# Kernel tuning notes

Measured on AMD Instinct MI355X. Metric: run time of the kernel, lower is better.

## Reference

```python
import jax, jax.numpy as jnp
import numpy as np

NUM_HEADS = 32
NUM_KV_HEADS = 8
HEAD_DIM = 128


def rotate_half(x):
    half = x.shape[-1] // 2
    return jnp.concatenate([-x[..., half:], x[..., :half]], axis=-1)


def setup_inputs() -> dict:
    key = jax.random.key(0)
    ks = jax.random.split(key, 7)
    B, S, H = 2, 2048, 4096
    hidden_states = jax.random.normal(ks[0], (B, S, H), dtype=jnp.float32)
    # rope tables built from real frequencies for realism
    inv_freq = 1.0 / (10000.0 ** (jnp.arange(0, HEAD_DIM, 2, dtype=jnp.float32) / HEAD_DIM))
    pos = jnp.arange(S, dtype=jnp.float32)
    freqs = pos[:, None] * inv_freq[None, :]            # [S, HEAD_DIM//2]
    emb = jnp.concatenate([freqs, freqs], axis=-1)      # [S, HEAD_DIM]
    cos = jnp.broadcast_to(jnp.cos(emb)[None], (B, S, HEAD_DIM)).astype(jnp.float32)
    sin = jnp.broadcast_to(jnp.sin(emb)[None], (B, S, HEAD_DIM)).astype(jnp.float32)
    scale = 0.02
    wq = jax.random.normal(ks[1], (NUM_HEADS * HEAD_DIM, H), dtype=jnp.float32) * scale
    wk = jax.random.normal(ks[2], (NUM_KV_HEADS * HEAD_DIM, H), dtype=jnp.float32) * scale
    wv = jax.random.normal(ks[3], (NUM_KV_HEADS * HEAD_DIM, H), dtype=jnp.float32) * scale
    wo = jax.random.normal(ks[4], (H, NUM_HEADS * HEAD_DIM), dtype=jnp.float32) * scale
    return {"hidden_states": hidden_states, "cos": cos, "sin": sin,
            "wq": wq, "wk": wk, "wv": wv, "wo": wo}


def reference(hidden_states, cos, sin, wq, wk, wv, wo):
    B, S, H = hidden_states.shape
    groups = NUM_HEADS // NUM_KV_HEADS
    scaling = HEAD_DIM ** -0.5

    # QKV projections (nn.Linear, no bias -> x @ W^T)
    q = (hidden_states @ wq.T).reshape(B, S, NUM_HEADS, HEAD_DIM).transpose(0, 2, 1, 3)     # [B,Hq,S,D]
    k = (hidden_states @ wk.T).reshape(B, S, NUM_KV_HEADS, HEAD_DIM).transpose(0, 2, 1, 3)  # [B,Hk,S,D]
    v = (hidden_states @ wv.T).reshape(B, S, NUM_KV_HEADS, HEAD_DIM).transpose(0, 2, 1, 3)  # [B,Hk,S,D]

    # RoPE (HF apply_rotary_pos_emb: cos/sin unsqueezed over head axis)
    c = cos[:, None, :, :]  # [B,1,S,D]
    s = sin[:, None, :, :]
    q = q * c + rotate_half(q) * s
    k = k * c + rotate_half(k) * s

    # GQA: broadcast each KV head to its group of query heads
    k = jnp.repeat(k, groups, axis=1)  # [B,Hq,S,D]
    v = jnp.repeat(v, groups, axis=1)

    # causal SDPA
    scores = jnp.einsum('bhqd,bhkd->bhqk', q, k) * scaling
    causal = jnp.tril(jnp.ones((S, S), dtype=bool))
    neg = jnp.finfo(scores.dtype).min
    scores = jnp.where(causal[None, None], scores, neg)
    probs = jax.nn.softmax(scores, axis=-1)
    attn = jnp.einsum('bhqk,bhkd->bhqd', probs, v)      # [B,Hq,S,D]

    # merge heads + output projection
    attn = attn.transpose(0, 2, 1, 3).reshape(B, S, NUM_HEADS * HEAD_DIM)
    return attn @ wo.T
```

## Files before the change

kernel.cpp:

```cpp
#include <hip/hip_runtime.h>
#include <stdint.h>

typedef __bf16 bf16_t;
typedef __bf16 bf16x8 __attribute__((ext_vector_type(8)));
typedef __bf16 bf16x4 __attribute__((ext_vector_type(4)));
typedef float f32x4 __attribute__((ext_vector_type(4)));

#define S_LEN 2048
#define NH 32
#define NKV 8
#define HD 128
#define B_SZ 2
#define HID 4096
#define QKV_N 6144
#define INFF __builtin_inff()
#define QSCALE (0.08838834764831845f * 1.4426950408889634f)

__device__ __forceinline__ void gload_lds16(const void* g, void* l) {
    __builtin_amdgcn_global_load_lds(
        (const __attribute__((address_space(1))) void*)(uintptr_t)g,
        (__attribute__((address_space(3))) void*)(uint32_t)(uintptr_t)l,
        16, 0, 0);
}

__global__ __launch_bounds__(256) void f2b_kernel(const float4* __restrict__ in,
                                                  bf16x4* __restrict__ out, int n4) {
    int i = blockIdx.x * blockDim.x + threadIdx.x;
    if (i >= n4) return;
    float4 v = in[i];
    bf16x4 o = {(bf16_t)v.x, (bf16_t)v.y, (bf16_t)v.z, (bf16_t)v.w};
    out[i] = o;
}

#define SLOT_E 16384

#define GTILE(T, STAGE, VMW) do {                                                         \
    const int _sb = ((T) & 3) * SLOT_E;                                                   \
    bf16x8 af[8], bfr[2];                                                                 \
    _Pragma("unroll") for (int i = 0; i < 8; ++i)                                         \
        af[i] = *(const bf16x8*)&lds[_sb + offA[i]];                                      \
    bfr[0] = *(const bf16x8*)&lds[_sb + 8192 + offB[0]];                                  \
    bfr[1] = *(const bf16x8*)&lds[_sb + 8192 + offB[1]];                                  \
    if (STAGE) {                                                                          \
        const int _ss = (((T) + 3) & 3) * SLOT_E;                                         \
        gload_lds16(sA0, &lds[_ss + ldsO0]); gload_lds16(sA1, &lds[_ss + ldsO1]);         \
        sA0 += 32; sA1 += 32;                                                             \
    }                                                                                     \
    __builtin_amdgcn_s_barrier();                                                         \
    asm volatile("s_waitcnt lgkmcnt(0)" ::: "memory");                                    \
    __builtin_amdgcn_sched_barrier(0);                                                    \
    __builtin_amdgcn_s_setprio(1);                                                        \
    _Pragma("unroll") for (int i = 0; i < 8; ++i) {                                       \
        acc[i][0] = __builtin_amdgcn_mfma_f32_16x16x32_bf16(af[i], bfr[0], acc[i][0], 0, 0, 0); \
        acc[i][1] = __builtin_amdgcn_mfma_f32_16x16x32_bf16(af[i], bfr[1], acc[i][1], 0, 0, 0); \
    }                                                                                     \
    __builtin_amdgcn_s_setprio(0);                                                        \
    __builtin_amdgcn_s_barrier();                                                         \
    bf16x8 bfs[2];                                                                        \
    bfs[0] = *(const bf16x8*)&lds[_sb + 8192 + offB[2]];                                  \
    bfs[1] = *(const bf16x8*)&lds[_sb + 8192 + offB[3]];                                  \
    if (STAGE) {                                                                          \
        const int _ss = (((T) + 3) & 3) * SLOT_E;                                         \
        gload_lds16(sB0, &lds[_ss + 8192 + ldsO0]); gload_lds16(sB1, &lds[_ss + 8192 + ldsO1]); \
        sB0 += 32; sB1 += 32;                                                             \
    }                                                                                     \
    __builtin_amdgcn_s_barrier();                                                         \
    asm volatile("s_waitcnt lgkmcnt(0)" ::: "memory");                                    \
    __builtin_amdgcn_sched_barrier(0);                                                    \
    __builtin_amdgcn_s_setprio(1);                                                        \
    _Pragma("unroll") for (int i = 0; i < 8; ++i) {                                       \
        acc[i][2] = __builtin_amdgcn_mfma_f32_16x16x32_bf16(af[i], bfs[0], acc[i][2], 0, 0, 0); \
        acc[i][3] = __builtin_amdgcn_mfma_f32_16x16x32_bf16(af[i], bfs[1], acc[i][3], 0, 0, 0); \
    }                                                                                     \
    __builtin_amdgcn_s_setprio(0);                                                        \
    if ((VMW) == 8)      asm volatile("s_waitcnt vmcnt(8)" ::: "memory");                 \
    else if ((VMW) == 4) asm volatile("s_waitcnt vmcnt(4)" ::: "memory");                 \
    else if ((VMW) == 0) asm volatile("s_waitcnt vmcnt(0)" ::: "memory");                 \
    __builtin_amdgcn_s_barrier();                                                         \
} while (0)

template<bool F32OUT>
__global__ __launch_bounds__(512, 2) void gemm256(const bf16_t* __restrict__ A,
                                                  const bf16_t* __restrict__ W,
                                                  void* __restrict__ C0,
                                                  void* __restrict__ C1,
                                                  int ld0, int ld1,
                                                  int Nloc, int ldAW, int Kloc) {
    __shared__ __align__(16) bf16_t lds[4 * SLOT_E];
    const int tid = threadIdx.x;
    const int lane = tid & 63;
    const int w = tid >> 6;
    const int wm = w >> 2, wn = w & 3;
    const int l15 = lane & 15, lg = lane >> 4;

    const int z = blockIdx.y;
    void* Cv = z ? C1 : C0;
    const int ldC = z ? ld1 : ld0;
    const int kOff = z * Kloc;

    const int nbx = Nloc >> 8;
    const int cpx = gridDim.x >> 3;
    const int bid = blockIdx.x;
    const int bid2 = (bid & 7) * cpx + (bid >> 3);
    const int m0 = (bid2 / nbx) * 256;
    const int n0 = (bid2 % nbx) * 256;

    const int c0 = tid, c1 = 512 + tid;
    const int rA0 = c0 >> 2, ch0 = (c0 & 3) ^ ((rA0 >> 1) & 3);
    const int rA1 = c1 >> 2, ch1 = (c1 & 3) ^ ((rA1 >> 1) & 3);
    const bf16_t* sA0 = A + (size_t)(m0 + rA0) * ldAW + kOff + ch0 * 8;
    const bf16_t* sA1 = A + (size_t)(m0 + rA1) * ldAW + kOff + ch1 * 8;
    const bf16_t* sB0 = W + (size_t)(n0 + rA0) * ldAW + kOff + ch0 * 8;
    const bf16_t* sB1 = W + (size_t)(n0 + rA1) * ldAW + kOff + ch1 * 8;
    const int ldsO0 = c0 * 8, ldsO1 = c1 * 8;

    int offA[8], offB[4];
    #pragma unroll
    for (int i = 0; i < 8; ++i) {
        int row = wm * 128 + i * 16 + l15;
        offA[i] = row * 32 + ((lg ^ ((row >> 1) & 3)) * 8);
    }
    #pragma unroll
    for (int j = 0; j < 4; ++j) {
        int row = wn * 64 + j * 16 + l15;
        offB[j] = row * 32 + ((lg ^ ((row >> 1) & 3)) * 8);
    }

    #pragma unroll
    for (int tt = 0; tt < 3; ++tt) {
        const int ss = tt * SLOT_E;
        gload_lds16(sA0, &lds[ss + ldsO0]); gload_lds16(sA1, &lds[ss + ldsO1]);
        gload_lds16(sB0, &lds[ss + 8192 + ldsO0]); gload_lds16(sB1, &lds[ss + 8192 + ldsO1]);
        sA0 += 32; sA1 += 32; sB0 += 32; sB1 += 32;
    }
    asm volatile("s_waitcnt vmcnt(8)" ::: "memory");
    __builtin_amdgcn_s_barrier();

    f32x4 acc[8][4] = {};
    const int NT = Kloc >> 5;
    int t = 0;
    for (; t < NT - 3; ++t) GTILE(t, true, 8);
    GTILE(NT - 3, false, 4);
    GTILE(NT - 2, false, 0);
    GTILE(NT - 1, false, -1);

    #pragma unroll
    for (int i = 0; i < 8; ++i)
        #pragma unroll
        for (int jn = 0; jn < 4; ++jn)
            #pragma unroll
            for (int r = 0; r < 4; ++r) {
                int m = m0 + wm * 128 + i * 16 + lg * 4 + r;
                int n = n0 + wn * 64 + jn * 16 + l15;
                float v = acc[i][jn][r];
                if (F32OUT) ((float*)Cv)[(size_t)m * ldC + n] = v;
                else        ((bf16_t*)Cv)[(size_t)m * ldC + n] = (bf16_t)v;
            }
}

__global__ __launch_bounds__(256) void rope_fuse(bf16_t* __restrict__ QKV,
                                                 const bf16_t* __restrict__ P1,
                                                 const float* __restrict__ cosb,
                                                 const float* __restrict__ sinb) {
    int tid = blockIdx.x * blockDim.x + threadIdx.x;
    int d = tid & 63;
    int hg = (tid >> 6) % 48;
    int bs = tid / (64 * 48);
    bf16_t* rowp;
    float x1, x2, posc = 1.f;
    if (hg < 32) {
        rowp = QKV + (size_t)bs * QKV_N + hg * HD;
        x1 = (float)rowp[d];
        x2 = (float)rowp[d + 64];
        posc = QSCALE;
    } else if (hg < 40) {
        int col = HID + (hg - 32) * HD;
        rowp = QKV + (size_t)bs * QKV_N + col;
        const bf16_t* pp = P1 + (size_t)bs * 2048 + (col - HID);
        x1 = (float)rowp[d] + (float)pp[d];
        x2 = (float)rowp[d + 64] + (float)pp[d + 64];
    } else {
        int col = HID + NKV * HD + (hg - 40) * HD;
        rowp = QKV + (size_t)bs * QKV_N + col;
        const bf16_t* pp = P1 + (size_t)bs * 2048 + (col - HID);
        rowp[d]      = (bf16_t)((float)rowp[d]      + (float)pp[d]);
        rowp[d + 64] = (bf16_t)((float)rowp[d + 64] + (float)pp[d + 64]);
        return;
    }
    float c1 = cosb[(size_t)bs * HD + d];
    float s1 = sinb[(size_t)bs * HD + d];
    float c2 = cosb[(size_t)bs * HD + d + 64];
    float s2 = sinb[(size_t)bs * HD + d + 64];
    rowp[d]      = (bf16_t)((x1 * c1 - x2 * s1) * posc);
    rowp[d + 64] = (bf16_t)((x2 * c2 + x1 * s2) * posc);
}

#define PITCH_P 72

__global__ __launch_bounds__(256, 3) void attn_fwd(const bf16_t* __restrict__ QKV,
                                                   bf16_t* __restrict__ O) {
    __shared__ __align__(16) bf16_t Kl[64 * 128];
    __shared__ __align__(16) bf16_t Vt[128 * 64];
    __shared__ __align__(16) bf16_t Pl[4][16 * PITCH_P];
    const int tid = threadIdx.x;
    const int lane = tid & 63;
    const int w = tid >> 6;
    const int l15 = lane & 15, lg = lane >> 4;
    const int pr = blockIdx.x, h = blockIdx.y, b = blockIdx.z;
    const int kvh = h >> 2;

    int krow[4], kch[4];
    for (int jj = 0; jj < 4; ++jj) { int q = jj * 256 + tid; krow[jj] = q >> 4; kch[jj] = q & 15; }
    const int d0 = (tid >> 4) * 8;
    const int k0v = (tid & 15) * 4;
    const int vci = k0v >> 3;
    const int vsub = k0v & 7;

    const bf16_t* Kb0 = QKV + (size_t)(b * S_LEN) * QKV_N + HID + kvh * HD;
    const bf16_t* Vb0 = QKV + (size_t)(b * S_LEN) * QKV_N + HID + NKV * HD + kvh * HD;
    bf16_t* Plw = Pl[w];

    for (int t = 0; t < 2; ++t) {
        const int qt = (t == 0) ? pr : (31 - pr);
        const int q0 = qt * 64;
        const int qrow = q0 + w * 16 + l15;

        bf16x8 qf[4];
        {
            const bf16_t* qp = QKV + (size_t)(b * S_LEN + qrow) * QKV_N + h * HD;
            #pragma unroll
            for (int c = 0; c < 4; ++c) qf[c] = *(const bf16x8*)&qp[c * 32 + lg * 8];
        }

        f32x4 acc_o[8] = {};
        float mrow = -INFF, lrow = 0.f;
        const int nsteps = qt + 1;

        bf16x8 kst[4], vst[4];
        #pragma unroll
        for (int jj = 0; jj < 4; ++jj)
            kst[jj] = *(const bf16x8*)&Kb0[(size_t)krow[jj] * QKV_N + kch[jj] * 8];
        #pragma unroll
        for (int j2 = 0; j2 < 4; ++j2)
            vst[j2] = *(const bf16x8*)&Vb0[(size_t)(k0v + j2) * QKV_N + d0];

        for (int st = 0; st < nsteps; ++st) {
            const int k0 = st * 64;
            __syncthreads();
            #pragma unroll
            for (int jj = 0; jj < 4; ++jj)
                *(bf16x8*)&Kl[krow[jj] * 128 + ((kch[jj] ^ (krow[jj] & 7)) * 8)] = kst[jj];
            #pragma unroll
            for (int j = 0; j < 8; ++j) {
                bf16x4 cvec = { vst[0][j], vst[1][j], vst[2][j], vst[3][j] };
                *(bf16x4*)&Vt[(d0 + j) * 64 + ((vci ^ j) << 3) + vsub] = cvec;
            }
            __syncthreads();
            if (st + 1 < nsteps) {
                const bf16_t* Kb = Kb0 + (size_t)(k0 + 64) * QKV_N;
                const bf16_t* Vb = Vb0 + (size_t)(k0 + 64) * QKV_N;
                #pragma unroll
                for (int jj = 0; jj < 4; ++jj)
                    kst[jj] = *(const bf16x8*)&Kb[(size_t)krow[jj] * QKV_N + kch[jj] * 8];
                #pragma unroll
                for (int j2 = 0; j2 < 4; ++j2)
                    vst[j2] = *(const bf16x8*)&Vb[(size_t)(k0v + j2) * QKV_N + d0];
            }
            f32x4 s[4];
            __builtin_amdgcn_s_setprio(1);
            #pragma unroll
            for (int nt = 0; nt < 4; ++nt) {
                s[nt] = (f32x4){0.f, 0.f, 0.f, 0.f};
                const int row = nt * 16 + l15;
                const int rb = row * 128, key = row & 7;
                #pragma unroll
                for (int c = 0; c < 4; ++c) {
                    bf16x8 kf = *(const bf16x8*)&Kl[rb + (((c * 4 + lg) ^ key) * 8)];
                    s[nt] = __builtin_amdgcn_mfma_f32_16x16x32_bf16(kf, qf[c], s[nt], 0, 0, 0);
                }
            }
            __builtin_amdgcn_s_setprio(0);
            if (k0 + 63 > q0 + w * 16) {
                #pragma unroll
                for (int nt = 0; nt < 4; ++nt)
                    #pragma unroll
                    for (int r = 0; r < 4; ++r) {
                        int k = k0 + nt * 16 + lg * 4 + r;
                        if (k > qrow) s[nt][r] = -INFF;
                    }
            }
            float m0a = fmaxf(fmaxf(s[0][0], s[0][1]), fmaxf(s[0][2], s[0][3]));
            float m1a = fmaxf(fmaxf(s[1][0], s[1][1]), fmaxf(s[1][2], s[1][3]));
            float m2a = fmaxf(fmaxf(s[2][0], s[2][1]), fmaxf(s[2][2], s[2][3]));
            float m3a = fmaxf(fmaxf(s[3][0], s[3][1]), fmaxf(s[3][2], s[3][3]));
            float mx = fmaxf(fmaxf(m0a, m1a), fmaxf(m2a, m3a));
            mx = fmaxf(mx, __shfl_xor(mx, 16));
            mx = fmaxf(mx, __shfl_xor(mx, 32));
            const bool nodefer = !__all(mx <= mrow + 11.5f);
            const float mn = nodefer ? fmaxf(mrow, mx) : mrow;
            float sc = 1.f;
            if (nodefer) sc = exp2f(mrow - mn);
            float rs0 = 0.f, rs1 = 0.f, rs2 = 0.f, rs3 = 0.f;
            #pragma unroll
            for (int nt = 0; nt < 4; ++nt) {
                float e0 = exp2f(s[nt][0] - mn), e1 = exp2f(s[nt][1] - mn);
                float e2 = exp2f(s[nt][2] - mn), e3 = exp2f(s[nt][3] - mn);
                s[nt][0] = e0; s[nt][1] = e1; s[nt][2] = e2; s[nt][3] = e3;
                rs0 += e0; rs1 += e1; rs2 += e2; rs3 += e3;
            }
            float rs = (rs0 + rs1) + (rs2 + rs3);
            rs += __shfl_xor(rs, 16);
            rs += __shfl_xor(rs, 32);
            if (nodefer) { lrow = lrow * sc + rs; mrow = mn; }
            else         { lrow += rs; }
            #pragma unroll
            for (int nt = 0; nt < 4; ++nt) {
                bf16x4 pk = {(bf16_t)s[nt][0], (bf16_t)s[nt][1], (bf16_t)s[nt][2], (bf16_t)s[nt][3]};
                *(bf16x4*)&Plw[l15 * PITCH_P + nt * 16 + lg * 4] = pk;
            }
            if (nodefer) {
                float scb[4];
                #pragma unroll
                for (int r = 0; r < 4; ++r) scb[r] = __shfl(sc, lg * 4 + r);
                #pragma unroll
                for (int nt2 = 0; nt2 < 8; ++nt2)
                    #pragma unroll
                    for (int r = 0; r < 4; ++r) acc_o[nt2][r] *= scb[r];
            }
            __builtin_amdgcn_s_setprio(1);
            #pragma unroll
            for (int kc = 0; kc < 2; ++kc) {
                bf16x8 pf = *(const bf16x8*)&Plw[l15 * PITCH_P + kc * 32 + lg * 8];
                #pragma unroll
                for (int nt2 = 0; nt2 < 8; ++nt2) {
                    const int drow = nt2 * 16 + l15;
                    bf16x8 vf = *(const bf16x8*)&Vt[drow * 64 + (((kc * 4 + lg) ^ (drow & 7)) << 3)];
                    acc_o[nt2] = __builtin_amdgcn_mfma_f32_16x16x32_bf16(pf, vf, acc_o[nt2], 0, 0, 0);
                }
            }
            __builtin_amdgcn_s_setprio(0);
        }
        float lb[4];
        #pragma unroll
        for (int r = 0; r < 4; ++r) lb[r] = __builtin_amdgcn_rcpf(__shfl(lrow, lg * 4 + r));
        #pragma unroll
        for (int nt2 = 0; nt2 < 8; ++nt2)
            #pragma unroll
            for (int r = 0; r < 4; ++r) {
                int q = q0 + w * 16 + lg * 4 + r;
                int d = nt2 * 16 + l15;
                O[((size_t)(b * S_LEN + q)) * (NH * HD) + h * HD + d] = (bf16_t)(acc_o[nt2][r] * lb[r]);
            }
    }
}

extern "C" void kernel_launch(void* const* d_in, const int* in_sizes, int n_in,
                              void* d_out, int out_size, void* d_ws, size_t ws_size,
                              hipStream_t stream) {
    const float* hs   = (const float*)d_in[0];
    const float* cosb = (const float*)d_in[1];
    const float* sinb = (const float*)d_in[2];
    const float* wq   = (const float*)d_in[3];
    const float* wk   = (const float*)d_in[4];
    const float* wv   = (const float*)d_in[5];
    const float* wo   = (const float*)d_in[6];
    float* out = (float*)d_out;

    const size_t NHS = (size_t)B_SZ * S_LEN * HID;
    const size_t NQKVW = (size_t)QKV_N * HID;
    size_t need = (NHS * 3 + NQKVW * 2) * sizeof(bf16_t);
    if (ws_size < need) return;

    bf16_t* p = (bf16_t*)d_ws;
    bf16_t* hsb  = p; p += NHS;
    bf16_t* wqkv = p; p += NQKVW;
    bf16_t* wob  = p; p += NHS;
    bf16_t* QKVb = p; p += NQKVW;
    bf16_t* Ab   = p; p += NHS;
    bf16_t* P1   = Ab;

    auto cvt = [&](const float* src, bf16_t* dst, size_t n) {
        int n4 = (int)(n / 4);
        f2b_kernel<<<(n4 + 255) / 256, 256, 0, stream>>>((const float4*)src, (bf16x4*)dst, n4);
    };
    cvt(hs, hsb, NHS);
    cvt(wq, wqkv, NHS);
    cvt(wk, wqkv + (size_t)HID * HID, (size_t)NKV * HD * HID);
    cvt(wv, wqkv + (size_t)(HID + NKV * HD) * HID, (size_t)NKV * HD * HID);
    cvt(wo, wob, NHS);

    gemm256<false><<<dim3(256, 1), 512, 0, stream>>>(hsb, wqkv, QKVb, QKVb,
                                                     QKV_N, QKV_N, 4096, HID, HID);
    gemm256<false><<<dim3(128, 2), 512, 0, stream>>>(hsb, wqkv + (size_t)HID * HID,
                                                     QKVb + HID, P1,
                                                     QKV_N, 2048, 2048, HID, 2048);

    int rf_threads = B_SZ * S_LEN * 48 * 64;
    rope_fuse<<<rf_threads / 256, 256, 0, stream>>>(QKVb, P1, cosb, sinb);

    attn_fwd<<<dim3(16, NH, B_SZ), 256, 0, stream>>>(QKVb, Ab);

    gemm256<true><<<dim3(256, 1), 512, 0, stream>>>(Ab, wob, out, out,
                                                    HID, HID, HID, HID, HID);
}
```

Before: 567.8 us.

## Share K/V tiles across the four GQA query heads in one attention block

```diff
diff --git a/kernel.cpp b/kernel.cpp
--- a/kernel.cpp
+++ b/kernel.cpp
@@ -4,6 +4,7 @@
 typedef __bf16 bf16_t;
 typedef __bf16 bf16x8 __attribute__((ext_vector_type(8)));
 typedef __bf16 bf16x4 __attribute__((ext_vector_type(4)));
+typedef __bf16 bf16x2 __attribute__((ext_vector_type(2)));
 typedef float f32x4 __attribute__((ext_vector_type(4)));
 
 #define S_LEN 2048
@@ -197,22 +198,24 @@
 
 #define PITCH_P 72
 
-__global__ __launch_bounds__(256, 3) void attn_fwd(const bf16_t* __restrict__ QKV,
+__global__ __launch_bounds__(512, 2) void attn_fwd(const bf16_t* __restrict__ QKV,
                                                    bf16_t* __restrict__ O) {
     __shared__ __align__(16) bf16_t Kl[64 * 128];
     __shared__ __align__(16) bf16_t Vt[128 * 64];
-    __shared__ __align__(16) bf16_t Pl[4][16 * PITCH_P];
+    __shared__ __align__(16) bf16_t Pl[8][16 * PITCH_P];
     const int tid = threadIdx.x;
     const int lane = tid & 63;
     const int w = tid >> 6;
     const int l15 = lane & 15, lg = lane >> 4;
-    const int pr = blockIdx.x, h = blockIdx.y, b = blockIdx.z;
-    const int kvh = h >> 2;
-
-    int krow[4], kch[4];
-    for (int jj = 0; jj < 4; ++jj) { int q = jj * 256 + tid; krow[jj] = q >> 4; kch[jj] = q & 15; }
-    const int d0 = (tid >> 4) * 8;
-    const int k0v = (tid & 15) * 4;
+    const int pr = blockIdx.x, kvh = blockIdx.y, b = blockIdx.z;
+    const int h = kvh * 4 + (w & 3);
+    const int rg = w >> 2;
+
+    int krow[2], kch[2];
+    #pragma unroll
+    for (int jj = 0; jj < 2; ++jj) { int q = jj * 512 + tid; krow[jj] = q >> 4; kch[jj] = q & 15; }
+    const int k0v = (tid & 31) * 2;
+    const int d0 = (tid >> 5) * 8;
     const int vci = k0v >> 3;
     const int vsub = k0v & 7;
 
@@ -221,9 +224,9 @@
     bf16_t* Plw = Pl[w];
 
     for (int t = 0; t < 2; ++t) {
-        const int qt = (t == 0) ? pr : (31 - pr);
-        const int q0 = qt * 64;
-        const int qrow = q0 + w * 16 + l15;
+        const int qt = (t == 0) ? pr : (63 - pr);
+        const int q0 = qt * 32;
+        const int qrow = q0 + rg * 16 + l15;
 
         bf16x8 qf[4];
         {
@@ -234,37 +237,35 @@
 
         f32x4 acc_o[8] = {};
         float mrow = -INFF, lrow = 0.f;
-        const int nsteps = qt + 1;
-
-        bf16x8 kst[4], vst[4];
+        const int nsteps = qt / 2 + 1;
+
+        bf16x8 kst[2], vst[2];
         #pragma unroll
-        for (int jj = 0; jj < 4; ++jj)
+        for (int jj = 0; jj < 2; ++jj)
             kst[jj] = *(const bf16x8*)&Kb0[(size_t)krow[jj] * QKV_N + kch[jj] * 8];
-        #pragma unroll
-        for (int j2 = 0; j2 < 4; ++j2)
-            vst[j2] = *(const bf16x8*)&Vb0[(size_t)(k0v + j2) * QKV_N + d0];
+        vst[0] = *(const bf16x8*)&Vb0[(size_t)(k0v + 0) * QKV_N + d0];
+        vst[1] = *(const bf16x8*)&Vb0[(size_t)(k0v + 1) * QKV_N + d0];
 
         for (int st = 0; st < nsteps; ++st) {
             const int k0 = st * 64;
             __syncthreads();
             #pragma unroll
-            for (int jj = 0; jj < 4; ++jj)
+            for (int jj = 0; jj < 2; ++jj)
                 *(bf16x8*)&Kl[krow[jj] * 128 + ((kch[jj] ^ (krow[jj] & 7)) * 8)] = kst[jj];
             #pragma unroll
             for (int j = 0; j < 8; ++j) {
-                bf16x4 cvec = { vst[0][j], vst[1][j], vst[2][j], vst[3][j] };
-                *(bf16x4*)&Vt[(d0 + j) * 64 + ((vci ^ j) << 3) + vsub] = cvec;
+                bf16x2 v2 = { vst[0][j], vst[1][j] };
+                *(bf16x2*)&Vt[(d0 + j) * 64 + ((vci ^ j) << 3) + vsub] = v2;
             }
             __syncthreads();
             if (st + 1 < nsteps) {
                 const bf16_t* Kb = Kb0 + (size_t)(k0 + 64) * QKV_N;
                 const bf16_t* Vb = Vb0 + (size_t)(k0 + 64) * QKV_N;
                 #pragma unroll
-                for (int jj = 0; jj < 4; ++jj)
+                for (int jj = 0; jj < 2; ++jj)
                     kst[jj] = *(const bf16x8*)&Kb[(size_t)krow[jj] * QKV_N + kch[jj] * 8];
-                #pragma unroll
-                for (int j2 = 0; j2 < 4; ++j2)
-                    vst[j2] = *(const bf16x8*)&Vb[(size_t)(k0v + j2) * QKV_N + d0];
+                vst[0] = *(const bf16x8*)&Vb[(size_t)(k0v + 0) * QKV_N + d0];
+                vst[1] = *(const bf16x8*)&Vb[(size_t)(k0v + 1) * QKV_N + d0];
             }
             f32x4 s[4];
             __builtin_amdgcn_s_setprio(1);
@@ -280,7 +281,7 @@
                 }
             }
             __builtin_amdgcn_s_setprio(0);
-            if (k0 + 63 > q0 + w * 16) {
+            if (k0 + 63 > q0 + rg * 16) {
                 #pragma unroll
                 for (int nt = 0; nt < 4; ++nt)
                     #pragma unroll
@@ -347,10 +348,11 @@
         for (int nt2 = 0; nt2 < 8; ++nt2)
             #pragma unroll
             for (int r = 0; r < 4; ++r) {
-                int q = q0 + w * 16 + lg * 4 + r;
+                int q = q0 + rg * 16 + lg * 4 + r;
                 int d = nt2 * 16 + l15;
                 O[((size_t)(b * S_LEN + q)) * (NH * HD) + h * HD + d] = (bf16_t)(acc_o[nt2][r] * lb[r]);
             }
+        __syncthreads();
     }
 }
 
@@ -398,7 +400,7 @@
     int rf_threads = B_SZ * S_LEN * 48 * 64;
     rope_fuse<<<rf_threads / 256, 256, 0, stream>>>(QKVb, P1, cosb, sinb);
 
-    attn_fwd<<<dim3(16, NH, B_SZ), 256, 0, stream>>>(QKVb, Ab);
+    attn_fwd<<<dim3(32, NKV, B_SZ), 512, 0, stream>>>(QKVb, Ab);
 
     gemm256<true><<<dim3(256, 1), 512, 0, stream>>>(Ab, wob, out, out,
                                                     HID, HID, HID, HID, HID);
```

After: 549.9 us. -3.2%, faster.
